# Kernel optimization log

Measured on AMD Instinct MI355X. Metric: run time of the kernel, lower is better.

The kernel has to match this reference:

```python
import jax, jax.numpy as jnp
import numpy as np

D_H = 2048      # d_hidden
D_E = 1408      # d_expert (per routed expert)
E = 8           # n_routed_experts
K = 2           # n_experts_per_token (top-k)
N_SHARED = 2    # n_shared_experts -> shared expert dim = D_E * N_SHARED
B, S = 1, 2048
D_S = D_E * N_SHARED


def setup_inputs() -> dict:
    key = jax.random.key(0)
    ks = jax.random.split(key, 8)
    def init(k, shape, fan_in):
        # nn.Linear default init: U(-1/sqrt(fan_in), 1/sqrt(fan_in))
        bound = 1.0 / np.sqrt(fan_in)
        return jax.random.uniform(k, shape, jnp.float32, -bound, bound)
    x = jax.random.normal(ks[0], (B, S, D_H), jnp.float32)
    gate_W = init(ks[1], (E, D_H), D_H)          # router: logits = x @ gate_W.T
    Wg_e = init(ks[2], (E, D_E, D_H), D_H)       # per-expert W_gate (out,in)
    Wu_e = init(ks[3], (E, D_E, D_H), D_H)       # per-expert W_up
    Wd_e = init(ks[4], (E, D_H, D_E), D_E)       # per-expert W_down
    Wg_s = init(ks[5], (D_S, D_H), D_H)          # shared expert W_gate
    Wu_s = init(ks[6], (D_S, D_H), D_H)
    Wd_s = init(ks[7], (D_H, D_S), D_S)
    return {"x": x, "gate_W": gate_W, "Wg_e": Wg_e, "Wu_e": Wu_e,
            "Wd_e": Wd_e, "Wg_s": Wg_s, "Wu_s": Wu_s, "Wd_s": Wd_s}


def reference(x, gate_W, Wg_e, Wu_e, Wd_e, Wg_s, Wu_s, Wd_s):
    silu = jax.nn.silu
    # shared expert: SiLU-gated MLP over all tokens
    shared = (silu(x @ Wg_s.T) * (x @ Wu_s.T)) @ Wd_s.T          # [B,S,D_H]
    # gating: softmax over experts, then top-k scores/indices
    scores = jax.nn.softmax(x @ gate_W.T, axis=-1)                # [B,S,E]
    topk_scores, topk_idx = jax.lax.top_k(scores, K)              # [B,S,K]
    # dense combine weights w[t,e] = topk score if e selected else 0
    # (equivalent to the torch argsort-dispatch + scatter_reduce sum combine)
    w = jnp.sum(jax.nn.one_hot(topk_idx, E, dtype=x.dtype) * topk_scores[..., None], axis=-2)  # [B,S,E]
    xf = x.reshape(-1, D_H)                                       # [T,D_H], T = B*S
    wf = w.reshape(-1, E)                                         # [T,E]
    # per-expert SiLU-gated MLP, batched over experts
    g = jnp.einsum('td,efd->etf', xf, Wg_e)                       # [E,T,D_E]
    u = jnp.einsum('td,efd->etf', xf, Wu_e)
    h = silu(g) * u
    oe = jnp.einsum('etf,edf->etd', h, Wd_e)                      # [E,T,D_H]
    routed = jnp.einsum('etd,te->td', oe, wf).reshape(B, S, D_H)
    return routed + shared
```

## Files before the change

kernel.cpp:

```cpp
#include <hip/hip_runtime.h>

using short8 = __attribute__((ext_vector_type(8))) short;
using f32x4  = __attribute__((ext_vector_type(4))) float;
typedef unsigned short ushort_t;
typedef unsigned int u32;

#define T_TOK 2048
#define DH 2048
#define DE 1408
#define DS 2816
#define GU_NB 440
#define DN_NB 256

#define NGEc 23068672UL
#define NGSc 5767168UL
#define NXc  4194304UL
#define PA_CVT_BLOCKS 7552
#define PB_CVT_BLOCKS 7040

#define FENCE() asm volatile("" ::: "memory")

__device__ __forceinline__ unsigned short f2bf(float f) {
  unsigned u = __float_as_uint(f);
  u += 0x7FFF + ((u >> 16) & 1);
  return (unsigned short)(u >> 16);
}

__device__ __forceinline__ float bf2f(short v) {
  return __uint_as_float(((u32)(unsigned short)v) << 16);
}

__device__ __forceinline__ void gl_lds16(const void* g, void* l) {
  __builtin_amdgcn_global_load_lds((const __attribute__((address_space(1))) u32*)g,
                                   (__attribute__((address_space(3))) u32*)l, 16, 0, 0);
}

__device__ __forceinline__ short8 pack_bf8(float4 a, float4 b) {
  short8 o;
  o[0] = (short)f2bf(a.x); o[1] = (short)f2bf(a.y);
  o[2] = (short)f2bf(a.z); o[3] = (short)f2bf(a.w);
  o[4] = (short)f2bf(b.x); o[5] = (short)f2bf(b.y);
  o[6] = (short)f2bf(b.z); o[7] = (short)f2bf(b.w);
  return o;
}

__global__ void phaseA_kernel(const float* __restrict__ x, const float* __restrict__ gW,
                              int* __restrict__ counts, int* __restrict__ tok_e,
                              int* __restrict__ tok_slot, float* __restrict__ tok_w,
                              const float* __restrict__ Wg_e, const float* __restrict__ Wu_e,
                              const float* __restrict__ Wg_s, const float* __restrict__ Wu_s,
                              ushort_t* wbg_e, ushort_t* wbu_e,
                              ushort_t* wbg_s, ushort_t* wbu_s, ushort_t* xb) {
  int b = blockIdx.x;
  int tid = threadIdx.x;
  if (b < 256) {
    int wid = tid >> 6, lane = tid & 63;
    int t = b * 8 + wid;
    float acc[8] = {0.f,0.f,0.f,0.f,0.f,0.f,0.f,0.f};
    const float* xt = x + (size_t)t * DH;
    for (int i = lane; i < DH; i += 64) {
      float xv = xt[i];
#pragma unroll
      for (int e = 0; e < 8; e++) acc[e] += xv * gW[e * DH + i];
    }
#pragma unroll
    for (int e = 0; e < 8; e++) {
#pragma unroll
      for (int off = 32; off > 0; off >>= 1) acc[e] += __shfl_xor(acc[e], off);
    }
    if (lane == 0) {
      float mx = acc[0];
      for (int e = 1; e < 8; e++) mx = fmaxf(mx, acc[e]);
      float p[8], se = 0.f;
      for (int e = 0; e < 8; e++) { p[e] = __expf(acc[e] - mx); se += p[e]; }
      for (int e = 0; e < 8; e++) p[e] /= se;
      int i1 = 0;
      for (int e = 1; e < 8; e++) if (p[e] > p[i1]) i1 = e;
      int i2 = (i1 == 0) ? 1 : 0;
      for (int e = 0; e < 8; e++) if (e != i1 && p[e] > p[i2]) i2 = e;
      int s1 = atomicAdd(&counts[i1], 1);
      int s2 = atomicAdd(&counts[i2], 1);
      tok_e[2 * t] = i1;     tok_e[2 * t + 1] = i2;
      tok_slot[2 * t] = s1;  tok_slot[2 * t + 1] = s2;
      tok_w[2 * t] = p[i1];  tok_w[2 * t + 1] = p[i2];
    }
    return;
  }
  size_t i = (size_t)(b - 256) * 8192 + (size_t)tid * 16;
  const float* s; ushort_t* d; size_t o;
  if      (i < NGEc)                    { s = Wg_e; d = wbg_e; o = i; }
  else if (i < 2 * NGEc)                { s = Wu_e; d = wbu_e; o = i - NGEc; }
  else if (i < 2 * NGEc + NGSc)         { s = Wg_s; d = wbg_s; o = i - 2 * NGEc; }
  else if (i < 2 * NGEc + 2 * NGSc)     { s = Wu_s; d = wbu_s; o = i - 2 * NGEc - NGSc; }
  else                                  { s = x;    d = xb;    o = i - 2 * NGEc - 2 * NGSc; }
  float4 a0 = *(const float4*)(s + o);
  float4 b0 = *(const float4*)(s + o + 4);
  float4 a1 = *(const float4*)(s + o + 8);
  float4 b1 = *(const float4*)(s + o + 12);
  *(short8*)(d + o)     = pack_bf8(a0, b0);
  *(short8*)(d + o + 8) = pack_bf8(a1, b1);
}

__global__ void prefix_assign_kernel(const int* __restrict__ counts, int* __restrict__ ebase,
                                     int* __restrict__ gu_off, int* __restrict__ dn_off,
                                     const int* __restrict__ tok_e, int* __restrict__ tok_slot,
                                     int* __restrict__ slot2tok) {
  __shared__ int sbase[8];
  if (threadIdx.x == 0) {
    int a = 0;
    for (int e = 0; e < 8; e++) { sbase[e] = a; ebase[e] = a; a += counts[e]; }
    int g = 0, d = 0;
    for (int z = 0; z < 8; z++) {
      gu_off[z] = g; dn_off[z] = d;
      int Lg = (counts[z] + 255) >> 8;
      g += Lg * 11;
      int Ld = (counts[z] + 255) >> 8;
      d += Ld * 8;
    }
    gu_off[8] = g; g += 88;
    gu_off[9] = g; g += 88;
    gu_off[10] = g;
    dn_off[8] = d; d += 64;
    dn_off[9] = d;
  }
  __syncthreads();
  for (int idx = threadIdx.x; idx < T_TOK * 2; idx += blockDim.x) {
    int e = tok_e[idx];
    int g = sbase[e] + tok_slot[idx];
    tok_slot[idx] = g;
    slot2tok[g] = idx >> 1;
  }
}

__global__ __launch_bounds__(512, 1) void phaseB_kernel(
    const ushort_t* __restrict__ xb, const int* __restrict__ counts,
    const int* __restrict__ ebase, const int* __restrict__ gu_off,
    const int* __restrict__ slot2tok,
    const ushort_t* __restrict__ Wbg_e, const ushort_t* __restrict__ Wbu_e,
    const ushort_t* __restrict__ Wbg_s, const ushort_t* __restrict__ Wbu_s,
    ushort_t* __restrict__ h_r, ushort_t* __restrict__ h_s,
    const float* __restrict__ Wd_e, const float* __restrict__ Wd_s,
    ushort_t* wbd_e, ushort_t* wbd_s) {
  extern __shared__ char smem[];
  int tid = threadIdx.x;
  if (blockIdx.x >= GU_NB) {
    size_t i = (size_t)(blockIdx.x - GU_NB) * 4096 + (size_t)tid * 8;
    const float* s; ushort_t* d; size_t o;
    if (i < NGEc) { s = Wd_e; d = wbd_e; o = i; }
    else          { s = Wd_s; d = wbd_s; o = i - NGEc; }
    float4 a = *(const float4*)(s + o);
    float4 bb = *(const float4*)(s + o + 4);
    *(short8*)(d + o) = pack_bf8(a, bb);
    return;
  }
  int b = blockIdx.x;
  int c = (b & 7) * (GU_NB >> 3) + (b >> 3);
  int off[11];
#pragma unroll
  for (int zz = 0; zz < 11; zz++) off[zz] = gu_off[zz];
  if (c >= off[10]) return;
  int z = 0;
#pragma unroll
  for (int zz = 1; zz < 10; zz++) if (c >= off[zz]) z = zz;
  int cz = c - off[z];

  bool routed = (z < 8);
  int cnt, gbase, Lm;
  const ushort_t *Bg, *Bu;
  if (routed) {
    cnt = counts[z]; gbase = ebase[z];
    Lm = (cnt + 255) >> 8;
    Bg = Wbg_e + (size_t)z * DE * DH;
    Bu = Wbu_e + (size_t)z * DE * DH;
  } else {
    cnt = T_TOK; gbase = 0; Lm = 8;
    Bg = Wbg_s + (size_t)(z - 8) * 1408 * DH;
    Bu = Wbu_s + (size_t)(z - 8) * 1408 * DH;
  }
  int mt = cz % Lm, y = cz / Lm;
  int m0 = mt * 256, n0 = y * 128;

  int lane = tid & 63, w = tid >> 6;
  int lr = lane & 15, lk = lane >> 4;
  int wm = w >> 1, wn = w & 1;

  const ushort_t* asrc[4];
  int adst[4];
#pragma unroll
  for (int j = 0; j < 4; j++) {
    int r = (w * 4 + j) * 8 + (lane >> 3);
    int lrow = m0 + r;
    int tok = routed ? ((lrow < cnt) ? slot2tok[gbase + lrow] : 0) : lrow;
    int cs = (lane & 7) ^ (r & 7);
    asrc[j] = xb + (size_t)tok * DH + cs * 8;
    adst[j] = (w * 4 + j) * 1024;
  }
  const ushort_t* gsrc[2];
  const ushort_t* usrc[2];
  int wdst[2];
#pragma unroll
  for (int j = 0; j < 2; j++) {
    int r = (w * 2 + j) * 8 + (lane >> 3);
    int cs = (lane & 7) ^ (r & 7);
    gsrc[j] = Bg + (size_t)(n0 + r) * DH + cs * 8;
    usrc[j] = Bu + (size_t)(n0 + r) * DH + cs * 8;
    wdst[j] = (w * 2 + j) * 1024;
  }

  f32x4 accg[4][4] = {};
  f32x4 accu[4][4] = {};

#define GU_STAGE(buf, k0)                                             \
  {                                                                   \
    char* ab = smem + (buf) * 32768;                                  \
    char* gb = smem + 65536 + (buf) * 16384;                          \
    char* ub = smem + 98304 + (buf) * 16384;                          \
    _Pragma("unroll")                                                 \
    for (int j = 0; j < 4; j++) gl_lds16(asrc[j] + (k0), ab + adst[j]); \
    _Pragma("unroll")                                                 \
    for (int j = 0; j < 2; j++) {                                     \
      gl_lds16(gsrc[j] + (k0), gb + wdst[j]);                         \
      gl_lds16(usrc[j] + (k0), ub + wdst[j]);                         \
    }                                                                 \
  }

  const int nt = DH >> 6;
  GU_STAGE(0, 0);
  __syncthreads();
  int cur = 0;
  for (int t = 0; t < nt; t++) {
    if (t + 1 < nt) GU_STAGE(cur ^ 1, (t + 1) * 64);
    const char* ab = smem + cur * 32768;
    const char* gb = smem + 65536 + cur * 16384;
    const char* ub = smem + 98304 + cur * 16384;
    short8 af[4][2], bg[4][2], bu[4][2];
#pragma unroll
    for (int m = 0; m < 4; m++) {
#pragma unroll
      for (int ks = 0; ks < 2; ks++) {
        int rr = wm * 64 + m * 16 + lr;
        af[m][ks] = *(const short8*)(ab + rr * 128 + ((ks * 64 + lk * 16) ^ ((rr & 7) << 4)));
      }
    }
#pragma unroll
    for (int n = 0; n < 4; n++) {
#pragma unroll
      for (int ks = 0; ks < 2; ks++) {
        int cc = wn * 64 + n * 16 + lr;
        bg[n][ks] = *(const short8*)(gb + cc * 128 + ((ks * 64 + lk * 16) ^ ((cc & 7) << 4)));
        bu[n][ks] = *(const short8*)(ub + cc * 128 + ((ks * 64 + lk * 16) ^ ((cc & 7) << 4)));
      }
    }
    __builtin_amdgcn_s_setprio(1);
#pragma unroll
    for (int m = 0; m < 4; m++) {
#pragma unroll
      for (int n = 0; n < 4; n++) {
#pragma unroll
        for (int ks = 0; ks < 2; ks++) {
          accg[m][n] = __builtin_amdgcn_mfma_f32_16x16x32_bf16(af[m][ks], bg[n][ks], accg[m][n], 0, 0, 0);
          accu[m][n] = __builtin_amdgcn_mfma_f32_16x16x32_bf16(af[m][ks], bu[n][ks], accu[m][n], 0, 0, 0);
        }
      }
    }
    __builtin_amdgcn_s_setprio(0);
    __syncthreads();
    cur ^= 1;
  }
#pragma unroll
  for (int m = 0; m < 4; m++) {
    int rowl = m0 + wm * 64 + m * 16 + lk * 4;
#pragma unroll
    for (int n = 0; n < 4; n++) {
      int col = n0 + wn * 64 + n * 16 + lr;
#pragma unroll
      for (int j = 0; j < 4; j++) {
        float g = accg[m][n][j], u = accu[m][n][j];
        float s = g / (1.f + __expf(-g));
        unsigned short hv = f2bf(s * u);
        if (routed) {
          if (rowl + j < cnt) h_r[(size_t)(gbase + rowl + j) * DE + col] = hv;
        } else {
          h_s[(size_t)(rowl + j) * DS + (z - 8) * 1408 + col] = hv;
        }
      }
    }
  }
}

__global__ __launch_bounds__(512, 1) void down_kernel(
    const ushort_t* __restrict__ h_r, const ushort_t* __restrict__ h_s,
    const int* __restrict__ counts, const int* __restrict__ ebase,
    const int* __restrict__ dn_off,
    const ushort_t* __restrict__ Wbd_e, const ushort_t* __restrict__ Wbd_s,
    ushort_t* __restrict__ oe, float* __restrict__ out) {
  extern __shared__ char smem[];

  int b = blockIdx.x;
  int c = (b & 7) * (DN_NB >> 3) + (b >> 3);
  int off[10];
#pragma unroll
  for (int zz = 0; zz < 10; zz++) off[zz] = dn_off[zz];
  if (c >= off[9]) return;
  int z = 0;
#pragma unroll
  for (int zz = 1; zz < 9; zz++) if (c >= off[zz]) z = zz;
  int cz = c - off[z];

  bool routed = (z < 8);
  int cnt, gbase, K, Lm;
  const ushort_t* Abase;
  const ushort_t* Bw;
  if (routed) {
    cnt = counts[z]; gbase = ebase[z];
    Lm = (cnt + 255) >> 8;
    K = DE;
    Abase = h_r + (size_t)gbase * DE;
    Bw = Wbd_e + (size_t)z * DH * DE;
  } else {
    cnt = T_TOK; gbase = 0; Lm = 8;
    K = DS;
    Abase = h_s;
    Bw = Wbd_s;
  }
  int mt = cz % Lm, y = cz / Lm;
  int m0 = mt * 256, n0 = y * 256;

  int tid = threadIdx.x;
  int lane = tid & 63, w = tid >> 6;
  int lr = lane & 15, lk = lane >> 4;
  int wm = w >> 2, wn = w & 3;

  const ushort_t* asrc[2][2];
  const ushort_t* bsrc[2][2];
  int sdst[2][2];
#pragma unroll
  for (int h = 0; h < 2; h++) {
#pragma unroll
    for (int j = 0; j < 2; j++) {
      int r = h * 128 + (w * 2 + j) * 8 + (lane >> 3);
      int cs = (lane & 7) ^ (r & 7);
      asrc[h][j] = Abase + (size_t)(m0 + r) * K + cs * 8;
      bsrc[h][j] = Bw + (size_t)(n0 + r) * K + cs * 8;
      sdst[h][j] = h * 16384 + (w * 2 + j) * 1024;
    }
  }

  f32x4 acc[8][4] = {};

#define DN_ST_A(p, h, k0)                                              \
  { char* _d = smem + (p) * 32768;                                     \
    gl_lds16(asrc[h][0] + (k0), _d + sdst[h][0]);                      \
    gl_lds16(asrc[h][1] + (k0), _d + sdst[h][1]); }
#define DN_ST_B(p, h, k0)                                              \
  { char* _d = smem + 65536 + (p) * 32768;                             \
    gl_lds16(bsrc[h][0] + (k0), _d + sdst[h][0]);                      \
    gl_lds16(bsrc[h][1] + (k0), _d + sdst[h][1]); }

  const int nt = K >> 6;
  DN_ST_A(0, 0, 0); DN_ST_A(0, 1, 0);
  DN_ST_B(0, 0, 0); DN_ST_B(0, 1, 0);
  DN_ST_B(1, 0, 64); DN_ST_B(1, 1, 64);
  asm volatile("s_waitcnt vmcnt(4)" ::: "memory");
  FENCE(); __builtin_amdgcn_s_barrier(); FENCE();

  short8 bfr[4][2];
  for (int t = 0; t < nt; t++) {
    int p = t & 1;
    const char* ab = smem + p * 32768;
    const char* bb = smem + 65536 + p * 32768;
    int k1 = (t + 1) * 64, k2 = (t + 2) * 64;
#pragma unroll
    for (int ph = 0; ph < 4; ph++) {
      if (ph == 0) {
#pragma unroll
        for (int n = 0; n < 4; n++) {
#pragma unroll
          for (int ks = 0; ks < 2; ks++) {
            int cc = wn * 64 + n * 16 + lr;
            bfr[n][ks] = *(const short8*)(bb + cc * 128 + ((ks * 64 + lk * 16) ^ ((cc & 7) << 4)));
          }
        }
      }
      short8 af[2][2];
#pragma unroll
      for (int m2 = 0; m2 < 2; m2++) {
#pragma unroll
        for (int ks = 0; ks < 2; ks++) {
          int rr = wm * 128 + ph * 32 + m2 * 16 + lr;
          af[m2][ks] = *(const short8*)(ab + rr * 128 + ((ks * 64 + lk * 16) ^ ((rr & 7) << 4)));
        }
      }
      if      (ph == 0) { if (t + 1 < nt) DN_ST_A(p ^ 1, 0, k1); }
      else if (ph == 1) { if (t + 1 < nt) DN_ST_A(p ^ 1, 1, k1); }
      else if (ph == 2) { if (t + 2 < nt) DN_ST_B(p, 0, k2); }
      else {
        if (t + 2 < nt) { DN_ST_B(p, 1, k2); asm volatile("s_waitcnt vmcnt(4)" ::: "memory"); }
        else            {                    asm volatile("s_waitcnt vmcnt(0)" ::: "memory"); }
      }
      FENCE(); __builtin_amdgcn_s_barrier(); FENCE();
      __builtin_amdgcn_s_setprio(1);
#pragma unroll
      for (int m2 = 0; m2 < 2; m2++) {
#pragma unroll
        for (int n = 0; n < 4; n++) {
#pragma unroll
          for (int ks = 0; ks < 2; ks++) {
            acc[ph * 2 + m2][n] = __builtin_amdgcn_mfma_f32_16x16x32_bf16(
                af[m2][ks], bfr[n][ks], acc[ph * 2 + m2][n], 0, 0, 0);
          }
        }
      }
      __builtin_amdgcn_s_setprio(0);
      FENCE(); __builtin_amdgcn_s_barrier(); FENCE();
    }
  }
#pragma unroll
  for (int m = 0; m < 8; m++) {
    int rowl = m0 + wm * 128 + m * 16 + lk * 4;
#pragma unroll
    for (int n = 0; n < 4; n++) {
      int col = n0 + wn * 64 + n * 16 + lr;
#pragma unroll
      for (int j = 0; j < 4; j++) {
        if (routed) {
          if (rowl + j < cnt)
            oe[(size_t)(gbase + rowl + j) * DH + col] = f2bf(acc[m][n][j]);
        } else {
          out[(size_t)(rowl + j) * DH + col] = acc[m][n][j];
        }
      }
    }
  }
}

__global__ void combine_kernel(const int* __restrict__ tok_gslot,
                               const float* __restrict__ tok_w,
                               const ushort_t* __restrict__ oe,
                               float* __restrict__ out) {
  int t = blockIdx.x;
  int g1 = tok_gslot[2 * t], g2 = tok_gslot[2 * t + 1];
  float w1 = tok_w[2 * t], w2 = tok_w[2 * t + 1];
  int i = threadIdx.x * 8;
  short8 a = *(const short8*)(oe + (size_t)g1 * DH + i);
  short8 b = *(const short8*)(oe + (size_t)g2 * DH + i);
  float4* po = (float4*)(out + (size_t)t * DH + i);
  float4 o0 = po[0], o1 = po[1];
  o0.x += w1 * bf2f(a[0]) + w2 * bf2f(b[0]);
  o0.y += w1 * bf2f(a[1]) + w2 * bf2f(b[1]);
  o0.z += w1 * bf2f(a[2]) + w2 * bf2f(b[2]);
  o0.w += w1 * bf2f(a[3]) + w2 * bf2f(b[3]);
  o1.x += w1 * bf2f(a[4]) + w2 * bf2f(b[4]);
  o1.y += w1 * bf2f(a[5]) + w2 * bf2f(b[5]);
  o1.z += w1 * bf2f(a[6]) + w2 * bf2f(b[6]);
  o1.w += w1 * bf2f(a[7]) + w2 * bf2f(b[7]);
  po[0] = o0; po[1] = o1;
}

extern "C" void kernel_launch(void* const* d_in, const int* in_sizes, int n_in,
                              void* d_out, int out_size, void* d_ws, size_t ws_size,
                              hipStream_t stream) {
  const float* x    = (const float*)d_in[0];
  const float* gW   = (const float*)d_in[1];
  const float* Wg_e = (const float*)d_in[2];
  const float* Wu_e = (const float*)d_in[3];
  const float* Wd_e = (const float*)d_in[4];
  const float* Wg_s = (const float*)d_in[5];
  const float* Wu_s = (const float*)d_in[6];
  const float* Wd_s = (const float*)d_in[7];
  float* out = (float*)d_out;

  char* ws = (char*)d_ws;
  int*   counts   = (int*)ws;
  int*   ebase    = (int*)(ws + 64);
  int*   gu_off   = (int*)(ws + 128);
  int*   dn_off   = (int*)(ws + 192);
  int*   tok_e    = (int*)(ws + 256);
  int*   tok_slot = (int*)(ws + 256 + 16384);
  float* tok_w    = (float*)(ws + 256 + 32768);
  int*   slot2tok = (int*)(ws + 256 + 49152);
  ushort_t* xb  = (ushort_t*)(ws + 131072);
  ushort_t* h_r = (ushort_t*)(ws + 131072 + (size_t)T_TOK * DH * 2);
  ushort_t* h_s = h_r + (size_t)4096 * DE;
  ushort_t* oe  = (ushort_t*)((char*)h_s + (size_t)T_TOK * DS * 2);
  ushort_t* wb  = (ushort_t*)((char*)oe + (size_t)4096 * DH * 4);
  ushort_t* wbg_e = wb;
  ushort_t* wbu_e = wb + NGEc;
  ushort_t* wbd_e = wb + 2 * NGEc;
  ushort_t* wbg_s = wb + 3 * NGEc;
  ushort_t* wbu_s = wbg_s + NGSc;
  ushort_t* wbd_s = wbg_s + 2 * NGSc;

  hipFuncSetAttribute((const void*)phaseB_kernel,
                      hipFuncAttributeMaxDynamicSharedMemorySize, 131072);
  hipFuncSetAttribute((const void*)down_kernel,
                      hipFuncAttributeMaxDynamicSharedMemorySize, 131072);

  hipMemsetAsync(counts, 0, 64, stream);
  phaseA_kernel<<<256 + PA_CVT_BLOCKS, 512, 0, stream>>>(
      x, gW, counts, tok_e, tok_slot, tok_w,
      Wg_e, Wu_e, Wg_s, Wu_s, wbg_e, wbu_e, wbg_s, wbu_s, xb);
  prefix_assign_kernel<<<1, 256, 0, stream>>>(counts, ebase, gu_off, dn_off,
                                              tok_e, tok_slot, slot2tok);
  phaseB_kernel<<<GU_NB + PB_CVT_BLOCKS, 512, 131072, stream>>>(
      xb, counts, ebase, gu_off, slot2tok, wbg_e, wbu_e, wbg_s, wbu_s, h_r, h_s,
      Wd_e, Wd_s, wbd_e, wbd_s);
  down_kernel<<<DN_NB, 512, 131072, stream>>>(
      h_r, h_s, counts, ebase, dn_off, wbd_e, wbd_s, oe, out);
  combine_kernel<<<T_TOK, 256, 0, stream>>>(tok_slot, tok_w, oe, out);
}
```

Baseline: 336.1 us.

## Restructure gate/up GEMM into phased 8-wave pipeline with LDS gate-up exchange

```diff
diff --git a/kernel.cpp b/kernel.cpp
--- a/kernel.cpp
+++ b/kernel.cpp
@@ -112,13 +112,12 @@
     int g = 0, d = 0;
     for (int z = 0; z < 8; z++) {
       gu_off[z] = g; dn_off[z] = d;
-      int Lg = (counts[z] + 255) >> 8;
-      g += Lg * 11;
-      int Ld = (counts[z] + 255) >> 8;
-      d += Ld * 8;
-    }
-    gu_off[8] = g; g += 88;
-    gu_off[9] = g; g += 88;
+      int L = (counts[z] + 255) >> 8;
+      g += L * 11;
+      d += L * 8;
+    }
+    gu_off[8] = g; g += 176;
+    gu_off[9] = g;
     gu_off[10] = g;
     dn_off[8] = d; d += 64;
     dn_off[9] = d;
@@ -165,123 +164,153 @@
   int cz = c - off[z];
 
   bool routed = (z < 8);
-  int cnt, gbase, Lm;
+  int cnt, gbase, Lm, hstride;
   const ushort_t *Bg, *Bu;
+  ushort_t* hdst;
   if (routed) {
     cnt = counts[z]; gbase = ebase[z];
     Lm = (cnt + 255) >> 8;
     Bg = Wbg_e + (size_t)z * DE * DH;
     Bu = Wbu_e + (size_t)z * DE * DH;
+    hdst = h_r + (size_t)gbase * DE;
+    hstride = DE;
   } else {
     cnt = T_TOK; gbase = 0; Lm = 8;
-    Bg = Wbg_s + (size_t)(z - 8) * 1408 * DH;
-    Bu = Wbu_s + (size_t)(z - 8) * 1408 * DH;
+    Bg = Wbg_s;
+    Bu = Wbu_s;
+    hdst = h_s;
+    hstride = DS;
   }
   int mt = cz % Lm, y = cz / Lm;
   int m0 = mt * 256, n0 = y * 128;
 
   int lane = tid & 63, w = tid >> 6;
   int lr = lane & 15, lk = lane >> 4;
-  int wm = w >> 1, wn = w & 1;
-
-  const ushort_t* asrc[4];
-  int adst[4];
-#pragma unroll
-  for (int j = 0; j < 4; j++) {
-    int r = (w * 4 + j) * 8 + (lane >> 3);
-    int lrow = m0 + r;
-    int tok = routed ? ((lrow < cnt) ? slot2tok[gbase + lrow] : 0) : lrow;
-    int cs = (lane & 7) ^ (r & 7);
-    asrc[j] = xb + (size_t)tok * DH + cs * 8;
-    adst[j] = (w * 4 + j) * 1024;
-  }
-  const ushort_t* gsrc[2];
-  const ushort_t* usrc[2];
-  int wdst[2];
-#pragma unroll
-  for (int j = 0; j < 2; j++) {
-    int r = (w * 2 + j) * 8 + (lane >> 3);
-    int cs = (lane & 7) ^ (r & 7);
-    gsrc[j] = Bg + (size_t)(n0 + r) * DH + cs * 8;
-    usrc[j] = Bu + (size_t)(n0 + r) * DH + cs * 8;
-    wdst[j] = (w * 2 + j) * 1024;
-  }
-
-  f32x4 accg[4][4] = {};
-  f32x4 accu[4][4] = {};
-
-#define GU_STAGE(buf, k0)                                             \
-  {                                                                   \
-    char* ab = smem + (buf) * 32768;                                  \
-    char* gb = smem + 65536 + (buf) * 16384;                          \
-    char* ub = smem + 98304 + (buf) * 16384;                          \
-    _Pragma("unroll")                                                 \
-    for (int j = 0; j < 4; j++) gl_lds16(asrc[j] + (k0), ab + adst[j]); \
-    _Pragma("unroll")                                                 \
-    for (int j = 0; j < 2; j++) {                                     \
-      gl_lds16(gsrc[j] + (k0), gb + wdst[j]);                         \
-      gl_lds16(usrc[j] + (k0), ub + wdst[j]);                         \
-    }                                                                 \
-  }
+  int wm = w >> 2, wn = w & 3;
+
+  const ushort_t* asrc[2][2];
+  const ushort_t* bsrc[2][2];
+  int sdst[2][2];
+#pragma unroll
+  for (int h = 0; h < 2; h++) {
+#pragma unroll
+    for (int j = 0; j < 2; j++) {
+      int rlow = (w * 2 + j) * 8 + (lane >> 3);
+      int r = h * 128 + rlow;
+      int cs = (lane & 7) ^ (r & 7);
+      int lrow = m0 + r;
+      int tok = routed ? ((lrow < cnt) ? slot2tok[gbase + lrow] : 0) : lrow;
+      asrc[h][j] = xb + (size_t)tok * DH + cs * 8;
+      bsrc[h][j] = (h == 0 ? Bg : Bu) + (size_t)(n0 + rlow) * DH + cs * 8;
+      sdst[h][j] = h * 16384 + (w * 2 + j) * 1024;
+    }
+  }
+
+  f32x4 acc[8][4] = {};
+
+#define GU_ST_A(p, h, k0)                                              \
+  { char* _d = smem + (p) * 32768;                                     \
+    gl_lds16(asrc[h][0] + (k0), _d + sdst[h][0]);                      \
+    gl_lds16(asrc[h][1] + (k0), _d + sdst[h][1]); }
+#define GU_ST_B(p, h, k0)                                              \
+  { char* _d = smem + 65536 + (p) * 32768;                             \
+    gl_lds16(bsrc[h][0] + (k0), _d + sdst[h][0]);                      \
+    gl_lds16(bsrc[h][1] + (k0), _d + sdst[h][1]); }
 
   const int nt = DH >> 6;
-  GU_STAGE(0, 0);
-  __syncthreads();
-  int cur = 0;
+  GU_ST_A(0, 0, 0); GU_ST_A(0, 1, 0);
+  GU_ST_B(0, 0, 0); GU_ST_B(0, 1, 0);
+  GU_ST_B(1, 0, 64); GU_ST_B(1, 1, 64);
+  asm volatile("s_waitcnt vmcnt(4)" ::: "memory");
+  FENCE(); __builtin_amdgcn_s_barrier(); FENCE();
+
+  short8 bfr[4][2];
   for (int t = 0; t < nt; t++) {
-    if (t + 1 < nt) GU_STAGE(cur ^ 1, (t + 1) * 64);
-    const char* ab = smem + cur * 32768;
-    const char* gb = smem + 65536 + cur * 16384;
-    const char* ub = smem + 98304 + cur * 16384;
-    short8 af[4][2], bg[4][2], bu[4][2];
-#pragma unroll
-    for (int m = 0; m < 4; m++) {
-#pragma unroll
-      for (int ks = 0; ks < 2; ks++) {
-        int rr = wm * 64 + m * 16 + lr;
-        af[m][ks] = *(const short8*)(ab + rr * 128 + ((ks * 64 + lk * 16) ^ ((rr & 7) << 4)));
-      }
-    }
-#pragma unroll
-    for (int n = 0; n < 4; n++) {
-#pragma unroll
-      for (int ks = 0; ks < 2; ks++) {
-        int cc = wn * 64 + n * 16 + lr;
-        bg[n][ks] = *(const short8*)(gb + cc * 128 + ((ks * 64 + lk * 16) ^ ((cc & 7) << 4)));
-        bu[n][ks] = *(const short8*)(ub + cc * 128 + ((ks * 64 + lk * 16) ^ ((cc & 7) << 4)));
-      }
-    }
-    __builtin_amdgcn_s_setprio(1);
-#pragma unroll
-    for (int m = 0; m < 4; m++) {
-#pragma unroll
-      for (int n = 0; n < 4; n++) {
+    int p = t & 1;
+    const char* ab = smem + p * 32768;
+    const char* bb = smem + 65536 + p * 32768;
+    int k1 = (t + 1) * 64, k2 = (t + 2) * 64;
+#pragma unroll
+    for (int ph = 0; ph < 4; ph++) {
+      if (ph == 0) {
+#pragma unroll
+        for (int n = 0; n < 4; n++) {
+#pragma unroll
+          for (int ks = 0; ks < 2; ks++) {
+            int cc = wn * 64 + n * 16 + lr;
+            bfr[n][ks] = *(const short8*)(bb + cc * 128 + ((ks * 64 + lk * 16) ^ ((cc & 7) << 4)));
+          }
+        }
+      }
+      short8 af[2][2];
+#pragma unroll
+      for (int m2 = 0; m2 < 2; m2++) {
 #pragma unroll
         for (int ks = 0; ks < 2; ks++) {
-          accg[m][n] = __builtin_amdgcn_mfma_f32_16x16x32_bf16(af[m][ks], bg[n][ks], accg[m][n], 0, 0, 0);
-          accu[m][n] = __builtin_amdgcn_mfma_f32_16x16x32_bf16(af[m][ks], bu[n][ks], accu[m][n], 0, 0, 0);
-        }
-      }
-    }
-    __builtin_amdgcn_s_setprio(0);
-    __syncthreads();
-    cur ^= 1;
-  }
-#pragma unroll
-  for (int m = 0; m < 4; m++) {
-    int rowl = m0 + wm * 64 + m * 16 + lk * 4;
-#pragma unroll
-    for (int n = 0; n < 4; n++) {
-      int col = n0 + wn * 64 + n * 16 + lr;
-#pragma unroll
-      for (int j = 0; j < 4; j++) {
-        float g = accg[m][n][j], u = accu[m][n][j];
-        float s = g / (1.f + __expf(-g));
-        unsigned short hv = f2bf(s * u);
-        if (routed) {
-          if (rowl + j < cnt) h_r[(size_t)(gbase + rowl + j) * DE + col] = hv;
-        } else {
-          h_s[(size_t)(rowl + j) * DS + (z - 8) * 1408 + col] = hv;
+          int rr = wm * 128 + ph * 32 + m2 * 16 + lr;
+          af[m2][ks] = *(const short8*)(ab + rr * 128 + ((ks * 64 + lk * 16) ^ ((rr & 7) << 4)));
+        }
+      }
+      if      (ph == 0) { if (t + 1 < nt) GU_ST_A(p ^ 1, 0, k1); }
+      else if (ph == 1) { if (t + 1 < nt) GU_ST_A(p ^ 1, 1, k1); }
+      else if (ph == 2) { if (t + 2 < nt) GU_ST_B(p, 0, k2); }
+      else {
+        if (t + 2 < nt) { GU_ST_B(p, 1, k2); asm volatile("s_waitcnt vmcnt(4)" ::: "memory"); }
+        else            {                    asm volatile("s_waitcnt vmcnt(0)" ::: "memory"); }
+      }
+      FENCE(); __builtin_amdgcn_s_barrier(); FENCE();
+      __builtin_amdgcn_s_setprio(1);
+#pragma unroll
+      for (int m2 = 0; m2 < 2; m2++) {
+#pragma unroll
+        for (int n = 0; n < 4; n++) {
+#pragma unroll
+          for (int ks = 0; ks < 2; ks++) {
+            acc[ph * 2 + m2][n] = __builtin_amdgcn_mfma_f32_16x16x32_bf16(
+                af[m2][ks], bfr[n][ks], acc[ph * 2 + m2][n], 0, 0, 0);
+          }
+        }
+      }
+      __builtin_amdgcn_s_setprio(0);
+      FENCE(); __builtin_amdgcn_s_barrier(); FENCE();
+    }
+  }
+
+  float* xch = (float*)smem;
+#pragma unroll
+  for (int pass = 0; pass < 2; pass++) {
+    FENCE(); __builtin_amdgcn_s_barrier(); FENCE();
+    if (wm == pass && wn >= 2) {
+#pragma unroll
+      for (int m = 0; m < 8; m++) {
+#pragma unroll
+        for (int n = 0; n < 4; n++) {
+#pragma unroll
+          for (int j = 0; j < 4; j++) {
+            int row = m * 16 + lk * 4 + j;
+            int col = (wn - 2) * 64 + n * 16 + lr;
+            xch[row * 132 + col] = acc[m][n][j];
+          }
+        }
+      }
+    }
+    FENCE(); __builtin_amdgcn_s_barrier(); FENCE();
+    if (wm == pass && wn < 2) {
+#pragma unroll
+      for (int m = 0; m < 8; m++) {
+#pragma unroll
+        for (int n = 0; n < 4; n++) {
+#pragma unroll
+          for (int j = 0; j < 4; j++) {
+            int row = m * 16 + lk * 4 + j;
+            int col = wn * 64 + n * 16 + lr;
+            float g = acc[m][n][j];
+            float u = xch[row * 132 + col];
+            float s = g / (1.f + __expf(-g));
+            int grow = m0 + pass * 128 + row;
+            if (!routed || grow < cnt)
+              hdst[(size_t)grow * hstride + n0 + col] = f2bf(s * u);
+          }
         }
       }
     }
```

New measurement: 356.4 us. 6.0% more time.
